# Kernel tuning notes

Measured on AMD Instinct MI355X. Metric: run time of the kernel, lower is better.

## Reference

```python
import jax, jax.numpy as jnp
import numpy as np

I_, J_, D_IN, D_H = 100, 8, 768, 64
N_NODES, N_HE, N_INC, N_CELLS, VOCAB = 160000, 320000, 1600000, 800, 30000
BN_EPS = 1e-5


def setup_inputs() -> dict:
    key = jax.random.key(0)
    ks = jax.random.split(key, 20)
    w = lambda k, s: jax.random.normal(k, s, jnp.float32) * 0.05
    inp = {}
    inp['x'] = jax.random.normal(ks[0], (I_, J_, D_IN), jnp.float32)
    inp['node_tokens'] = jax.random.randint(ks[1], (N_NODES,), 0, VOCAB)
    inp['inc_node'] = jax.random.randint(ks[2], (N_INC,), 0, N_NODES)
    inp['inc_hedge'] = jnp.sort(jax.random.randint(ks[3], (N_INC,), 0, N_HE))
    inp['node2cell'] = jnp.sort(jax.random.randint(ks[4], (N_NODES,), 0, N_CELLS))
    inp['vac_emb'] = w(ks[5], (VOCAB, D_IN))
    inp['fhi_w'] = w(ks[6], (D_IN, D_H)); inp['fhi_b'] = jnp.zeros((D_H,), jnp.float32)
    inp['fin_w'] = w(ks[7], (D_IN, D_H)); inp['fin_b'] = jnp.zeros((D_H,), jnp.float32)
    inp['th1'] = w(ks[8], (D_H, D_H)); inp['b1'] = jnp.zeros((D_H,), jnp.float32)
    inp['th2'] = w(ks[9], (D_H, D_H)); inp['b2'] = jnp.zeros((D_H,), jnp.float32)
    for li, k in zip((1, 2, 3), (ks[10], ks[11], ks[12])):
        inp[f'wc{li}'] = w(k, (D_H, D_H, 3))
        inp[f'bc{li}'] = jnp.zeros((D_H,), jnp.float32)
        inp[f'g{li}'] = jnp.ones((D_H,), jnp.float32)
        inp[f'be{li}'] = jnp.zeros((D_H,), jnp.float32)
        inp[f'm{li}'] = jnp.zeros((D_H,), jnp.float32)
        inp[f'v{li}'] = jnp.ones((D_H,), jnp.float32)
    inp['fct_w'] = w(ks[13], (D_H, D_H)); inp['fct_b'] = jnp.zeros((D_H,), jnp.float32)
    return inp


def _inv_safe(c):
    return jnp.where(c > 0, 1.0 / jnp.maximum(c, 1.0), 0.0)


def _hconv(xf, inc_node, inc_hedge, theta, bias):
    # PyG HypergraphConv (no attention): D^{-1} H W B^{-1} H^T (X Theta) + bias
    xt = xf @ theta                                        # [N, D]
    ones = jnp.ones((inc_node.shape[0],), xt.dtype)
    deg_e = jax.ops.segment_sum(ones, inc_hedge, N_HE)     # B_e
    he = jax.ops.segment_sum(xt[inc_node], inc_hedge, N_HE) * _inv_safe(deg_e)[:, None]
    deg_v = jax.ops.segment_sum(ones, inc_node, N_NODES)   # D_v
    out = jax.ops.segment_sum(he[inc_hedge], inc_node, N_NODES) * _inv_safe(deg_v)[:, None]
    return out + bias


def _conv_bn(h, wc, bc, g, be, m, v):
    # Conv1d(k=3, pad=1) -> ReLU -> BatchNorm1d (inference stats); dropout is eval-mode identity
    h = jax.lax.conv_general_dilated(h, wc, (1,), [(1, 1)],
                                     dimension_numbers=('NCH', 'OIH', 'NCH')) + bc[None, :, None]
    h = jax.nn.relu(h)
    return (h - m[None, :, None]) * (g[None, :, None] / jnp.sqrt(v[None, :, None] + BN_EPS)) + be[None, :, None]


def _forward(x, node_tokens, inc_node, inc_hedge, node2cell, vac_emb, fhi_w, fhi_b,
             fin_w, fin_b, th1, b1, th2, b2, wc1, bc1, g1, be1, m1, v1,
             wc2, bc2, g2, be2, m2, v2, wc3, bc3, g3, be3, m3, v3, fct_w, fct_b):
    # x = fin(x)
    x0 = jnp.einsum('ijd,dh->ijh', x, fin_w) + fin_b       # [100, 8, 64]
    # node_features = fhi(graph_embedding[graph.x])  (gather-dominated)
    nf = vac_emb[node_tokens] @ fhi_w + fhi_b              # [N, 64]
    # two HypergraphConv layers with residuals (eval-mode dropout = identity)
    h1 = jax.nn.relu(_hconv(nf, inc_node, inc_hedge, th1, b1)) + nf
    gx = jax.nn.relu(_hconv(h1, inc_node, inc_hedge, th2, b2)) + nf
    # per-graph mean + max pooling (graph.batch is all-zero per graph => one vector per cell)
    cnt = jax.ops.segment_sum(jnp.ones((N_NODES,), gx.dtype), node2cell, N_CELLS)
    mean_p = jax.ops.segment_sum(gx, node2cell, N_CELLS) * _inv_safe(cnt)[:, None]
    max_p = jax.ops.segment_max(gx, node2cell, N_CELLS)
    max_p = jnp.where(cnt[:, None] > 0, max_p, 0.0)
    cell_emb = 0.5 * (mean_p + max_p)                      # [800, 64]
    x_upd = x0 + 0.3 * cell_emb.reshape(I_, J_, D_H)       # x[i,j] += 0.3*graph_emb
    h = jnp.transpose(x_upd, (0, 2, 1))                    # [100, 64, 8]
    h = _conv_bn(h, wc1, bc1, g1, be1, m1, v1)
    h = _conv_bn(h, wc2, bc2, g2, be2, m2, v2)
    h = _conv_bn(h, wc3, bc3, g3, be3, m3, v3)
    out2 = jnp.mean(h, axis=2) @ fct_w + fct_b             # [100, 64]
    return x_upd, out2


def reference(x, node_tokens, inc_node, inc_hedge, node2cell, vac_emb, fhi_w, fhi_b,
              fin_w, fin_b, th1, b1, th2, b2, wc1, bc1, g1, be1, m1, v1,
              wc2, bc2, g2, be2, m2, v2, wc3, bc3, g3, be3, m3, v3, fct_w, fct_b):
    return _forward(x, node_tokens, inc_node, inc_hedge, node2cell, vac_emb, fhi_w, fhi_b,
                    fin_w, fin_b, th1, b1, th2, b2, wc1, bc1, g1, be1, m1, v1,
                    wc2, bc2, g2, be2, m2, v2, wc3, bc3, g3, be3, m3, v3, fct_w, fct_b)
```

## Files before the change

kernel.cpp:

```cpp
#include <hip/hip_runtime.h>
#include <hip/hip_bf16.h>
#include <cstdint>
#include <cstddef>

#define I_      100
#define J_      8
#define D_IN    768
#define D_H     64
#define N_NODES 160000
#define N_HE    320000
#define N_INC   1600000
#define N_CELLS 800
#define VOCAB   30000

#define NRANGE   256
#define NPR      625
#define SLAB     8192
#define NCHUNK   1000
#define EPB      (N_INC / NCHUNK)

typedef unsigned short u16;
using short8 = __attribute__((ext_vector_type(8))) short;
using f32x4  = __attribute__((ext_vector_type(4))) float;

__device__ __forceinline__ float bf2f(u16 u) {
    union { uint32_t i; float f; } x; x.i = ((uint32_t)u) << 16; return x.f;
}
__device__ __forceinline__ u16 f2bf(float f) {
    union { float f; uint32_t i; } x; x.f = f;
    uint32_t b = x.i;
    b += 0x7FFFu + ((b >> 16) & 1u);
    return (u16)(b >> 16);
}
__device__ __forceinline__ float lo_bf(uint32_t u) {
    union { uint32_t i; float f; } x; x.i = u << 16; return x.f;
}
__device__ __forceinline__ float hi_bf(uint32_t u) {
    union { uint32_t i; float f; } x; x.i = u & 0xFFFF0000u; return x.f;
}
__device__ __forceinline__ uint32_t pack_bf2(float a, float b) {
    return (uint32_t)f2bf(a) | ((uint32_t)f2bf(b) << 16);
}

#define G_OFF_HE   (N_INC / 256)
#define G_OFF_CELL (N_NODES / 256)
#define G_CONV_BIG ((D_IN * 64) / 256)
#define G_CONV_SM  ((64 * 64) / 256)
#define G_KA       NCHUNK
#define G_KB1      256
#define G_KC       NCHUNK
#define G_KD       256
#define G_PGEMM    ((VOCAB + 63) / 64)
#define G_XT       (N_NODES / 64)
#define G_X0       ((I_ * J_ + 63) / 64)
#define G_HEDGE    (N_HE / 32)
#define G_NODE     (N_NODES / 32)

__device__ __forceinline__ void dev_offsets(int bid, const int* __restrict__ sorted,
                                            int n, int nbins, int* __restrict__ off) {
    int i = bid * 256 + threadIdx.x;
    if (i >= n) return;
    int cur = sorted[i];
    int prev = (i == 0) ? -1 : sorted[i - 1];
    for (int b = prev + 1; b <= cur; ++b) off[b] = i;
    if (i == n - 1) {
        for (int b = cur + 1; b <= nbins; ++b) off[b] = n;
    }
}

__device__ __forceinline__ void dev_convT(int bid, const float* __restrict__ B,
                                          u16* __restrict__ Bt, int K) {
    int g = bid * 256 + threadIdx.x;
    if (g >= K * 64) return;
    int k = g >> 6, n = g & 63;
    Bt[(size_t)n * K + k] = f2bf(B[g]);
}

__device__ __forceinline__ void dev_ka(int bid, const int* __restrict__ inc_node,
                                       int* __restrict__ counts, int* __restrict__ lds) {
    int tid = threadIdx.x;
    lds[tid] = 0;
    __syncthreads();
    int s = bid * EPB, e = s + EPB;
    for (int i = s + tid; i < e; i += 256)
        atomicAdd(&lds[(unsigned)inc_node[i] / NPR], 1);
    __syncthreads();
    counts[bid * NRANGE + tid] = lds[tid];
}

__device__ __forceinline__ void dev_kb1(int r, const int* __restrict__ counts,
                                        int* __restrict__ chunk_off,
                                        int* __restrict__ range_total,
                                        int* __restrict__ lds) {
    int tid = threadIdx.x;
    int c0 = tid * 4;
    int v0 = (c0     < NCHUNK) ? counts[(c0    ) * NRANGE + r] : 0;
    int v1 = (c0 + 1 < NCHUNK) ? counts[(c0 + 1) * NRANGE + r] : 0;
    int v2 = (c0 + 2 < NCHUNK) ? counts[(c0 + 2) * NRANGE + r] : 0;
    int v3 = (c0 + 3 < NCHUNK) ? counts[(c0 + 3) * NRANGE + r] : 0;
    int s = v0 + v1 + v2 + v3;
    lds[tid] = s;
    __syncthreads();
    #pragma unroll
    for (int d = 1; d < 256; d <<= 1) {
        int t = (tid >= d) ? lds[tid - d] : 0;
        __syncthreads();
        lds[tid] += t;
        __syncthreads();
    }
    int run = lds[tid] - s;
    if (c0     < NCHUNK) { chunk_off[(c0    ) * NRANGE + r] = run; run += v0; }
    if (c0 + 1 < NCHUNK) { chunk_off[(c0 + 1) * NRANGE + r] = run; run += v1; }
    if (c0 + 2 < NCHUNK) { chunk_off[(c0 + 2) * NRANGE + r] = run; run += v2; }
    if (c0 + 3 < NCHUNK) { chunk_off[(c0 + 3) * NRANGE + r] = run; run += v3; }
    if (tid == 255) range_total[r] = lds[255];
}

__device__ __forceinline__ void dev_kc(int bid, const int* __restrict__ inc_node,
                                       const int* __restrict__ inc_hedge,
                                       const int* __restrict__ chunk_off,
                                       int2* __restrict__ bucket, int* __restrict__ lds) {
    int tid = threadIdx.x;
    int* co  = lds;
    int* cur = lds + 256;
    co[tid]  = tid * SLAB + chunk_off[bid * NRANGE + tid];
    cur[tid] = 0;
    __syncthreads();
    int s = bid * EPB, e = s + EPB;
    for (int i = s + tid; i < e; i += 256) {
        int v = inc_node[i];
        int h = inc_hedge[i];
        int rg = (unsigned)v / NPR;
        int rank = atomicAdd(&cur[rg], 1);
        bucket[co[rg] + rank] = make_int2(v, h);
    }
}

__device__ __forceinline__ void dev_kd(int r, const int2* __restrict__ bucket,
                                       const int* __restrict__ range_total,
                                       int* __restrict__ node_off, int* __restrict__ node_deg,
                                       int* __restrict__ csr, int* __restrict__ lds) {
    int tid = threadIdx.x;
    int* hist = lds;
    int* tsum = lds + 768;
    int* cur  = lds + 1024;
    for (int i = tid; i < 768; i += 256) { hist[i] = 0; cur[i] = 0; }
    __syncthreads();
    int lo = r * NPR;
    int pb = r * SLAB;
    int pe = pb + range_total[r];
    for (int i = pb + tid; i < pe; i += 256)
        atomicAdd(&hist[bucket[i].x - lo], 1);
    __syncthreads();
    int b3 = tid * 3;
    int a0 = hist[b3], a1 = hist[b3 + 1], a2 = hist[b3 + 2];
    int s = a0 + a1 + a2;
    tsum[tid] = s;
    __syncthreads();
    #pragma unroll
    for (int d = 1; d < 256; d <<= 1) {
        int t = (tid >= d) ? tsum[tid - d] : 0;
        __syncthreads();
        tsum[tid] += t;
        __syncthreads();
    }
    int excl = tsum[tid] - s;
    hist[b3]     = excl;
    hist[b3 + 1] = excl + a0;
    hist[b3 + 2] = excl + a0 + a1;
    __syncthreads();
    for (int v = tid; v < NPR; v += 256) {
        int h0 = hist[v];
        node_off[lo + v] = pb + h0;
        node_deg[lo + v] = hist[v + 1] - h0;
    }
    for (int i = pb + tid; i < pe; i += 256) {
        int2 p = bucket[i];
        int l = p.x - lo;
        int k = atomicAdd(&cur[l], 1);
        csr[pb + hist[l] + k] = p.y;
    }
}

template <int BF16_OUT, int GATHER, int KK>
__device__ __forceinline__ void dev_gemm_direct(int wid, const float* __restrict__ A,
                                                const int* __restrict__ tok,
                                                const u16* __restrict__ Bt,
                                                const float* __restrict__ bias,
                                                void* __restrict__ C, int M) {
    int lane = threadIdx.x & 63;
    int m16 = lane & 15, q = lane >> 4;
    int base = wid << 4;
    if (base >= M) return;
    int row = base + m16;
    const float* arow = GATHER ? (A + ((size_t)tok[row] << 6))
                               : (A + (size_t)row * KK);

    f32x4 acc0 = {0.f, 0.f, 0.f, 0.f};
    f32x4 acc1 = {0.f, 0.f, 0.f, 0.f};
    f32x4 acc2 = {0.f, 0.f, 0.f, 0.f};
    f32x4 acc3 = {0.f, 0.f, 0.f, 0.f};

    #pragma unroll 2
    for (int kt = 0; kt < KK; kt += 32) {
        const float* ap = arow + kt + q * 8;
        float4 av0 = *reinterpret_cast<const float4*>(ap);
        float4 av1 = *reinterpret_cast<const float4*>(ap + 4);
        short8 a;
        a[0] = (short)f2bf(av0.x); a[1] = (short)f2bf(av0.y);
        a[2] = (short)f2bf(av0.z); a[3] = (short)f2bf(av0.w);
        a[4] = (short)f2bf(av1.x); a[5] = (short)f2bf(av1.y);
        a[6] = (short)f2bf(av1.z); a[7] = (short)f2bf(av1.w);
        const u16* bp = Bt + (size_t)m16 * KK + kt + q * 8;
        short8 b0 = *reinterpret_cast<const short8*>(bp);
        short8 b1 = *reinterpret_cast<const short8*>(bp + (size_t)16 * KK);
        short8 b2 = *reinterpret_cast<const short8*>(bp + (size_t)32 * KK);
        short8 b3 = *reinterpret_cast<const short8*>(bp + (size_t)48 * KK);
        acc0 = __builtin_amdgcn_mfma_f32_16x16x32_bf16(a, b0, acc0, 0, 0, 0);
        acc1 = __builtin_amdgcn_mfma_f32_16x16x32_bf16(a, b1, acc1, 0, 0, 0);
        acc2 = __builtin_amdgcn_mfma_f32_16x16x32_bf16(a, b2, acc2, 0, 0, 0);
        acc3 = __builtin_amdgcn_mfma_f32_16x16x32_bf16(a, b3, acc3, 0, 0, 0);
    }

    f32x4 accs[4] = {acc0, acc1, acc2, acc3};
    #pragma unroll
    for (int r = 0; r < 4; ++r) {
        int gr = base + q * 4 + r;
        #pragma unroll
        for (int j = 0; j < 4; ++j) {
            int col = j * 16 + m16;
            float v = accs[j][r];
            if (!BF16_OUT) v += bias[col];
            if (BF16_OUT)
                ((u16*)C)[(size_t)gr * 64 + col] = f2bf(v);
            else
                ((float*)C)[(size_t)gr * 64 + col] = v;
        }
    }
}

__device__ __forceinline__ void dev_hedge_sum(int bid, const int* __restrict__ inc_node,
                                              const int* __restrict__ he_off,
                                              const u16* __restrict__ xt,
                                              u16* __restrict__ he) {
    int w = (bid * 256 + (int)threadIdx.x) >> 6;
    int lane = threadIdx.x & 63;
    int sub = lane >> 3;
    int c8 = (lane & 7) << 3;
    int hedge = w * 8 + sub;
    if (hedge >= N_HE) return;
    int s = he_off[hedge], e = he_off[hedge + 1];

    float a0 = 0.f, a1 = 0.f, a2 = 0.f, a3 = 0.f;
    float a4 = 0.f, a5 = 0.f, a6 = 0.f, a7 = 0.f;
    float b0 = 0.f, b1 = 0.f, b2 = 0.f, b3 = 0.f;
    float b4 = 0.f, b5 = 0.f, b6 = 0.f, b7 = 0.f;

    int j = s;
    if ((e - s) & 1) {
        uint4 d = *reinterpret_cast<const uint4*>(xt + (((size_t)inc_node[j]) << 6) + c8);
        a0 += lo_bf(d.x); a1 += hi_bf(d.x);
        a2 += lo_bf(d.y); a3 += hi_bf(d.y);
        a4 += lo_bf(d.z); a5 += hi_bf(d.z);
        a6 += lo_bf(d.w); a7 += hi_bf(d.w);
        ++j;
    }
    int i0 = 0, i1 = 0;
    if (j < e) { i0 = inc_node[j]; i1 = inc_node[j + 1]; }
    for (; j < e; j += 2) {
        int c0 = i0, c1 = i1;
        if (j + 2 < e) { i0 = inc_node[j + 2]; i1 = inc_node[j + 3]; }
        uint4 d0 = *reinterpret_cast<const uint4*>(xt + (((size_t)c0) << 6) + c8);
        uint4 d1 = *reinterpret_cast<const uint4*>(xt + (((size_t)c1) << 6) + c8);
        a0 += lo_bf(d0.x); a1 += hi_bf(d0.x);
        a2 += lo_bf(d0.y); a3 += hi_bf(d0.y);
        a4 += lo_bf(d0.z); a5 += hi_bf(d0.z);
        a6 += lo_bf(d0.w); a7 += hi_bf(d0.w);
        b0 += lo_bf(d1.x); b1 += hi_bf(d1.x);
        b2 += lo_bf(d1.y); b3 += hi_bf(d1.y);
        b4 += lo_bf(d1.z); b5 += hi_bf(d1.z);
        b6 += lo_bf(d1.w); b7 += hi_bf(d1.w);
    }
    a0 += b0; a1 += b1; a2 += b2; a3 += b3;
    a4 += b4; a5 += b5; a6 += b6; a7 += b7;

    float inv = (e > s) ? 1.f / (float)(e - s) : 0.f;
    uint4 o;
    o.x = pack_bf2(a0 * inv, a1 * inv);
    o.y = pack_bf2(a2 * inv, a3 * inv);
    o.z = pack_bf2(a4 * inv, a5 * inv);
    o.w = pack_bf2(a6 * inv, a7 * inv);
    *reinterpret_cast<uint4*>(he + (((size_t)hedge) << 6) + c8) = o;
}

__device__ __forceinline__ void dev_node_sum(int bid, const int* __restrict__ csr,
                                             const int* __restrict__ node_off,
                                             const int* __restrict__ node_deg,
                                             const u16* __restrict__ he,
                                             const float* __restrict__ bias,
                                             const float* __restrict__ P,
                                             const int* __restrict__ tok,
                                             float* __restrict__ out) {
    int w = (bid * 256 + (int)threadIdx.x) >> 6;
    int lane = threadIdx.x & 63;
    int sub = lane >> 3;
    int c8 = (lane & 7) << 3;
    int node = w * 8 + sub;
    if (node >= N_NODES) return;
    int s = node_off[node];
    int e = s + node_deg[node];

    float a0 = 0.f, a1 = 0.f, a2 = 0.f, a3 = 0.f;
    float a4 = 0.f, a5 = 0.f, a6 = 0.f, a7 = 0.f;
    float b0 = 0.f, b1 = 0.f, b2 = 0.f, b3 = 0.f;
    float b4 = 0.f, b5 = 0.f, b6 = 0.f, b7 = 0.f;

    int j = s;
    if ((e - s) & 1) {
        uint4 d = *reinterpret_cast<const uint4*>(he + (((size_t)csr[j]) << 6) + c8);
        a0 += lo_bf(d.x); a1 += hi_bf(d.x);
        a2 += lo_bf(d.y); a3 += hi_bf(d.y);
        a4 += lo_bf(d.z); a5 += hi_bf(d.z);
        a6 += lo_bf(d.w); a7 += hi_bf(d.w);
        ++j;
    }
    int i0 = 0, i1 = 0;
    if (j < e) { i0 = csr[j]; i1 = csr[j + 1]; }
    for (; j < e; j += 2) {
        int c0 = i0, c1 = i1;
        if (j + 2 < e) { i0 = csr[j + 2]; i1 = csr[j + 3]; }
        uint4 d0 = *reinterpret_cast<const uint4*>(he + (((size_t)c0) << 6) + c8);
        uint4 d1 = *reinterpret_cast<const uint4*>(he + (((size_t)c1) << 6) + c8);
        a0 += lo_bf(d0.x); a1 += hi_bf(d0.x);
        a2 += lo_bf(d0.y); a3 += hi_bf(d0.y);
        a4 += lo_bf(d0.z); a5 += hi_bf(d0.z);
        a6 += lo_bf(d0.w); a7 += hi_bf(d0.w);
        b0 += lo_bf(d1.x); b1 += hi_bf(d1.x);
        b2 += lo_bf(d1.y); b3 += hi_bf(d1.y);
        b4 += lo_bf(d1.z); b5 += hi_bf(d1.z);
        b6 += lo_bf(d1.w); b7 += hi_bf(d1.w);
    }
    a0 += b0; a1 += b1; a2 += b2; a3 += b3;
    a4 += b4; a5 += b5; a6 += b6; a7 += b7;

    float inv = (e > s) ? 1.f / (float)(e - s) : 0.f;
    const float* nfp = P + (((size_t)tok[node]) << 6) + c8;
    float4 nv0 = *reinterpret_cast<const float4*>(nfp);
    float4 nv1 = *reinterpret_cast<const float4*>(nfp + 4);
    float4 o0, o1;
    o0.x = fmaxf(fmaf(a0, inv, bias[c8 + 0]), 0.f) + nv0.x;
    o0.y = fmaxf(fmaf(a1, inv, bias[c8 + 1]), 0.f) + nv0.y;
    o0.z = fmaxf(fmaf(a2, inv, bias[c8 + 2]), 0.f) + nv0.z;
    o0.w = fmaxf(fmaf(a3, inv, bias[c8 + 3]), 0.f) + nv0.w;
    o1.x = fmaxf(fmaf(a4, inv, bias[c8 + 4]), 0.f) + nv1.x;
    o1.y = fmaxf(fmaf(a5, inv, bias[c8 + 5]), 0.f) + nv1.y;
    o1.z = fmaxf(fmaf(a6, inv, bias[c8 + 6]), 0.f) + nv1.z;
    o1.w = fmaxf(fmaf(a7, inv, bias[c8 + 7]), 0.f) + nv1.w;
    float* op = out + (((size_t)node) << 6) + c8;
    *reinterpret_cast<float4*>(op) = o0;
    *reinterpret_cast<float4*>(op + 4) = o1;
}

__global__ __launch_bounds__(256) void k_p0(const float* __restrict__ fhi_w,
                                            const float* __restrict__ fin_w,
                                            const float* __restrict__ th1,
                                            const float* __restrict__ th2,
                                            u16* __restrict__ Bt_fhi, u16* __restrict__ Bt_fin,
                                            u16* __restrict__ Bt_th1, u16* __restrict__ Bt_th2,
                                            const int* __restrict__ inc_node,
                                            int* __restrict__ counts) {
    __shared__ int lds[256];
    int bid = blockIdx.x;
    if (bid < G_KA) { dev_ka(bid, inc_node, counts, lds); return; }
    bid -= G_KA;
    if (bid < G_CONV_BIG) { dev_convT(bid, fhi_w, Bt_fhi, D_IN); return; }
    bid -= G_CONV_BIG;
    if (bid < G_CONV_BIG) { dev_convT(bid, fin_w, Bt_fin, D_IN); return; }
    bid -= G_CONV_BIG;
    if (bid < G_CONV_SM) { dev_convT(bid, th1, Bt_th1, 64); return; }
    bid -= G_CONV_SM;
    dev_convT(bid, th2, Bt_th2, 64);
}

__global__ __launch_bounds__(256) void k_p1(const float* __restrict__ vac_emb,
                                            const u16* __restrict__ Bt_fhi,
                                            const float* __restrict__ fhi_b, float* __restrict__ P,
                                            const int* __restrict__ counts,
                                            int* __restrict__ chunk_off, int* __restrict__ range_total,
                                            const int* __restrict__ inc_hedge,
                                            const int* __restrict__ node2cell,
                                            int* __restrict__ he_off, int* __restrict__ cell_off) {
    __shared__ int lds[256];
    int bid = blockIdx.x;
    if (bid < G_KB1) { dev_kb1(bid, counts, chunk_off, range_total, lds); return; }
    bid -= G_KB1;
    if (bid < G_PGEMM) {
        int wid = bid * 4 + ((int)threadIdx.x >> 6);
        dev_gemm_direct<0, 0, D_IN>(wid, vac_emb, nullptr, Bt_fhi, fhi_b, P, VOCAB);
        return;
    }
    bid -= G_PGEMM;
    if (bid < G_OFF_HE) { dev_offsets(bid, inc_hedge, N_INC, N_HE, he_off); return; }
    bid -= G_OFF_HE;
    dev_offsets(bid, node2cell, N_NODES, N_CELLS, cell_off);
}

__global__ __launch_bounds__(256) void k_p2(const float* __restrict__ P,
                                            const int* __restrict__ tok,
                                            const u16* __restrict__ Bt_th1, u16* __restrict__ xt,
                                            const float* __restrict__ x, const u16* __restrict__ Bt_fin,
                                            const float* __restrict__ fin_b, float* __restrict__ x0,
                                            const int* __restrict__ inc_node,
                                            const int* __restrict__ inc_hedge,
                                            const int* __restrict__ chunk_off,
                                            int2* __restrict__ bucket) {
    __shared__ int lds[512];
    int bid = blockIdx.x;
    if (bid < G_KC) { dev_kc(bid, inc_node, inc_hedge, chunk_off, bucket, lds); return; }
    bid -= G_KC;
    if (bid < G_XT) {
        int wid = bid * 4 + ((int)threadIdx.x >> 6);
        dev_gemm_direct<1, 1, 64>(wid, P, tok, Bt_th1, nullptr, xt, N_NODES);
        return;
    }
    bid -= G_XT;
    {
        int wid = bid * 4 + ((int)threadIdx.x >> 6);
        dev_gemm_direct<0, 0, D_IN>(wid, x, nullptr, Bt_fin, fin_b, x0, I_ * J_);
    }
}

__global__ __launch_bounds__(256) void k_p3(const int* __restrict__ inc_node,
                                            const int* __restrict__ he_off,
                                            const u16* __restrict__ xt, u16* __restrict__ he,
                                            const int2* __restrict__ bucket,
                                            const int* __restrict__ range_total,
                                            int* __restrict__ node_off, int* __restrict__ node_deg,
                                            int* __restrict__ csr) {
    __shared__ int lds[1792];
    int bid = blockIdx.x;
    if (bid < G_KD) { dev_kd(bid, bucket, range_total, node_off, node_deg, csr, lds); return; }
    bid -= G_KD;
    dev_hedge_sum(bid, inc_node, he_off, xt, he);
}

__global__ __launch_bounds__(256) void k_xt2(const float* __restrict__ A,
                                             const u16* __restrict__ Bt,
                                             u16* __restrict__ xt) {
    int wid = blockIdx.x * 4 + ((int)threadIdx.x >> 6);
    dev_gemm_direct<1, 0, 64>(wid, A, nullptr, Bt, nullptr, xt, N_NODES);
}

__global__ __launch_bounds__(256) void k_hedge_sum(const int* __restrict__ inc_node,
                                                   const int* __restrict__ he_off,
                                                   const u16* __restrict__ xt,
                                                   u16* __restrict__ he) {
    dev_hedge_sum(blockIdx.x, inc_node, he_off, xt, he);
}

__global__ __launch_bounds__(256) void k_node_sum(const int* __restrict__ csr,
                                                  const int* __restrict__ node_off,
                                                  const int* __restrict__ node_deg,
                                                  const u16* __restrict__ he,
                                                  const float* __restrict__ bias,
                                                  const float* __restrict__ P,
                                                  const int* __restrict__ tok,
                                                  float* __restrict__ out) {
    dev_node_sum(blockIdx.x, csr, node_off, node_deg, he, bias, P, tok, out);
}

__global__ __launch_bounds__(256) void k_pool(const float* __restrict__ gx,
                                              const int* __restrict__ cell_off,
                                              const float* __restrict__ x0,
                                              float* __restrict__ out1) {
    __shared__ float ssum[4][64];
    __shared__ float smax[4][64];
    int c = blockIdx.x;
    int lane = threadIdx.x & 63;
    int w = threadIdx.x >> 6;
    int s = cell_off[c], e = cell_off[c + 1];
    float sum = 0.f, mx = -INFINITY;
    for (int n = s + w; n < e; n += 4) {
        float v = gx[((size_t)n << 6) + lane];
        sum += v;
        mx = fmaxf(mx, v);
    }
    ssum[w][lane] = sum;
    smax[w][lane] = mx;
    __syncthreads();
    if (w == 0) {
        sum = ssum[0][lane] + ssum[1][lane] + ssum[2][lane] + ssum[3][lane];
        mx = fmaxf(fmaxf(smax[0][lane], smax[1][lane]), fmaxf(smax[2][lane], smax[3][lane]));
        int cnt = e - s;
        float mean = (cnt > 0) ? sum / (float)cnt : 0.f;
        float mp = (cnt > 0) ? mx : 0.f;
        float ce = 0.5f * (mean + mp);
        out1[((size_t)c << 6) + lane] = x0[((size_t)c << 6) + lane] + 0.3f * ce;
    }
}

__global__ __launch_bounds__(256) void k_tcn(
    const float* __restrict__ xu,
    const float* __restrict__ wc1, const float* __restrict__ bc1, const float* __restrict__ g1,
    const float* __restrict__ be1, const float* __restrict__ m1, const float* __restrict__ v1,
    const float* __restrict__ wc2, const float* __restrict__ bc2, const float* __restrict__ g2,
    const float* __restrict__ be2, const float* __restrict__ m2, const float* __restrict__ v2,
    const float* __restrict__ wc3, const float* __restrict__ bc3, const float* __restrict__ g3,
    const float* __restrict__ be3, const float* __restrict__ m3, const float* __restrict__ v3,
    const float* __restrict__ fct_w, const float* __restrict__ fct_b,
    float* __restrict__ out2) {
    __shared__ float w_lds[64 * 64 * 3];
    __shared__ float hA[64][10];
    __shared__ float hB[64][10];
    __shared__ float mo[64];

    int n = blockIdx.x, tid = threadIdx.x;

    if (tid < 64) {
        hA[tid][0] = 0.f; hA[tid][9] = 0.f;
        hB[tid][0] = 0.f; hB[tid][9] = 0.f;
    }
    #pragma unroll
    for (int l = tid; l < 512; l += 256) {
        int t = l >> 6, i = l & 63;
        hA[i][t + 1] = xu[(size_t)n * 512 + l];
    }

    const float* wcs[3] = {wc1, wc2, wc3};
    const float* bcs[3] = {bc1, bc2, bc3};
    const float* gs[3]  = {g1, g2, g3};
    const float* bes[3] = {be1, be2, be3};
    const float* ms[3]  = {m1, m2, m3};
    const float* vs[3]  = {v1, v2, v3};

    float (*hin)[10] = hA;
    float (*hout)[10] = hB;

    #pragma unroll
    for (int li = 0; li < 3; ++li) {
        for (int l = tid; l < 64 * 64 * 3; l += 256) w_lds[l] = wcs[li][l];
        __syncthreads();
        #pragma unroll
        for (int rep = 0; rep < 2; ++rep) {
            int idx = tid + rep * 256;
            int o = idx >> 3, t = idx & 7;
            float acc = bcs[li][o];
            #pragma unroll 8
            for (int i = 0; i < 64; ++i) {
                const float* wr = &w_lds[o * 192 + i * 3];
                acc = fmaf(hin[i][t + 0], wr[0], acc);
                acc = fmaf(hin[i][t + 1], wr[1], acc);
                acc = fmaf(hin[i][t + 2], wr[2], acc);
            }
            acc = fmaxf(acc, 0.f);
            float sc = gs[li][o] * rsqrtf(vs[li][o] + 1e-5f);
            acc = (acc - ms[li][o]) * sc + bes[li][o];
            hout[o][t + 1] = acc;
        }
        __syncthreads();
        float (*tmp)[10] = hin; hin = hout; hout = tmp;
    }

    if (tid < 64) {
        float s = 0.f;
        #pragma unroll
        for (int t = 0; t < 8; ++t) s += hin[tid][t + 1];
        mo[tid] = s * 0.125f;
    }
    __syncthreads();
    if (tid < 64) {
        float acc = fct_b[tid];
        #pragma unroll 8
        for (int o = 0; o < 64; ++o) acc = fmaf(mo[o], fct_w[o * 64 + tid], acc);
        out2[(size_t)n * 64 + tid] = acc;
    }
}

extern "C" void kernel_launch(void* const* d_in, const int* in_sizes, int n_in,
                              void* d_out, int out_size, void* d_ws, size_t ws_size,
                              hipStream_t stream) {
    (void)in_sizes; (void)n_in; (void)out_size; (void)ws_size;

    const float* x          = (const float*)d_in[0];
    const int*   node_tok   = (const int*)d_in[1];
    const int*   inc_node   = (const int*)d_in[2];
    const int*   inc_hedge  = (const int*)d_in[3];
    const int*   node2cell  = (const int*)d_in[4];
    const float* vac_emb    = (const float*)d_in[5];
    const float* fhi_w      = (const float*)d_in[6];
    const float* fhi_b      = (const float*)d_in[7];
    const float* fin_w      = (const float*)d_in[8];
    const float* fin_b      = (const float*)d_in[9];
    const float* th1        = (const float*)d_in[10];
    const float* b1         = (const float*)d_in[11];
    const float* th2        = (const float*)d_in[12];
    const float* b2         = (const float*)d_in[13];
    const float* fct_w      = (const float*)d_in[32];
    const float* fct_b      = (const float*)d_in[33];

    char* ws = (char*)d_ws;
    size_t off = 0;
    float* P        = (float*)(ws + off); off += (size_t)VOCAB * 64 * 4;
    float* hbuf     = (float*)(ws + off); off += (size_t)N_NODES * 64 * 4;
    u16*   xt       = (u16*)(ws + off);   off += (size_t)N_NODES * 64 * 2;
    u16*   he       = (u16*)(ws + off);   off += (size_t)N_HE * 64 * 2;
    int2*  bucket   = (int2*)(ws + off);  off += (size_t)NRANGE * SLAB * 8;
    int*   csr      = (int*)(ws + off);   off += (size_t)NRANGE * SLAB * 4;
    float* x0       = (float*)(ws + off); off += (size_t)N_CELLS * 64 * 4;
    u16*   Bt_fhi   = (u16*)(ws + off);   off += (size_t)64 * D_IN * 2;
    u16*   Bt_fin   = (u16*)(ws + off);   off += (size_t)64 * D_IN * 2;
    u16*   Bt_th1   = (u16*)(ws + off);   off += (size_t)64 * 64 * 2;
    u16*   Bt_th2   = (u16*)(ws + off);   off += (size_t)64 * 64 * 2;
    int*   he_off   = (int*)(ws + off);   off += ((size_t)(N_HE + 1) * 4 + 255) / 256 * 256;
    int*   node_off = (int*)(ws + off);   off += (size_t)N_NODES * 4;
    int*   node_deg = (int*)(ws + off);   off += (size_t)N_NODES * 4;
    int*   cell_off = (int*)(ws + off);   off += ((size_t)(N_CELLS + 1) * 4 + 255) / 256 * 256;

    int*  counts      = (int*)hbuf;
    int*  chunk_off   = counts + NCHUNK * NRANGE;
    int*  range_total = chunk_off + NCHUNK * NRANGE;

    float* out1 = (float*)d_out;
    float* out2 = out1 + (size_t)I_ * J_ * D_H;

    k_p0<<<G_KA + 2 * G_CONV_BIG + 2 * G_CONV_SM, 256, 0, stream>>>(
        fhi_w, fin_w, th1, th2, Bt_fhi, Bt_fin, Bt_th1, Bt_th2,
        inc_node, counts);

    k_p1<<<G_KB1 + G_PGEMM + G_OFF_HE + G_OFF_CELL, 256, 0, stream>>>(
        vac_emb, Bt_fhi, fhi_b, P, counts, chunk_off, range_total,
        inc_hedge, node2cell, he_off, cell_off);

    k_p2<<<G_KC + G_XT + G_X0, 256, 0, stream>>>(
        P, node_tok, Bt_th1, xt, x, Bt_fin, fin_b, x0,
        inc_node, inc_hedge, chunk_off, bucket);

    k_p3<<<G_KD + G_HEDGE, 256, 0, stream>>>(inc_node, he_off, xt, he,
                                             bucket, range_total, node_off, node_deg, csr);

    k_node_sum<<<G_NODE, 256, 0, stream>>>(csr, node_off, node_deg, he, b1, P, node_tok, hbuf);

    k_xt2<<<G_XT, 256, 0, stream>>>(hbuf, Bt_th2, xt);

    k_hedge_sum<<<G_HEDGE, 256, 0, stream>>>(inc_node, he_off, xt, he);

    k_node_sum<<<G_NODE, 256, 0, stream>>>(csr, node_off, node_deg, he, b2, P, node_tok, hbuf);

    k_pool<<<N_CELLS, 256, 0, stream>>>(hbuf, cell_off, x0, out1);

    k_tcn<<<I_, 256, 0, stream>>>(out1,
        (const float*)d_in[14], (const float*)d_in[15], (const float*)d_in[16],
        (const float*)d_in[17], (const float*)d_in[18], (const float*)d_in[19],
        (const float*)d_in[20], (const float*)d_in[21], (const float*)d_in[22],
        (const float*)d_in[23], (const float*)d_in[24], (const float*)d_in[25],
        (const float*)d_in[26], (const float*)d_in[27], (const float*)d_in[28],
        (const float*)d_in[29], (const float*)d_in[30], (const float*)d_in[31],
        fct_w, fct_b, out2);
}
```

Before: 502.8 us.

## Fuse first node aggregation with theta2 GEMM and fold pooling into TCN kernel

The first node-sum now packs its 32 rows per block into LDS as bf16 and runs the 64x64 theta2 projection with MFMA in the same kernel, writing xt directly. This skips the fp32 hbuf round trip and the separate GEMM launch. Cell pooling (mean+max) also moves into the TCN kernel, which removes the k_pool launch. The catch is that the pooling loop now runs serially per wave over about 200 nodes per cell with only 100 blocks, so that phase has much less parallelism than the 800-block pool kernel it replaces.

```diff
diff --git a/kernel.cpp b/kernel.cpp
--- a/kernel.cpp
+++ b/kernel.cpp
@@ -55,6 +55,7 @@
 #define G_X0       ((I_ * J_ + 63) / 64)
 #define G_HEDGE    (N_HE / 32)
 #define G_NODE     (N_NODES / 32)
+#define G_NXT      (N_NODES / 32)
 
 __device__ __forceinline__ void dev_offsets(int bid, const int* __restrict__ sorted,
                                             int n, int nbins, int* __restrict__ off) {
@@ -293,20 +294,14 @@
     *reinterpret_cast<uint4*>(he + (((size_t)hedge) << 6) + c8) = o;
 }
 
-__device__ __forceinline__ void dev_node_sum(int bid, const int* __restrict__ csr,
-                                             const int* __restrict__ node_off,
-                                             const int* __restrict__ node_deg,
-                                             const u16* __restrict__ he,
-                                             const float* __restrict__ bias,
-                                             const float* __restrict__ P,
-                                             const int* __restrict__ tok,
-                                             float* __restrict__ out) {
-    int w = (bid * 256 + (int)threadIdx.x) >> 6;
-    int lane = threadIdx.x & 63;
-    int sub = lane >> 3;
-    int c8 = (lane & 7) << 3;
-    int node = w * 8 + sub;
-    if (node >= N_NODES) return;
+__device__ __forceinline__ void dev_node_core(int node, const int* __restrict__ csr,
+                                              const int* __restrict__ node_off,
+                                              const int* __restrict__ node_deg,
+                                              const u16* __restrict__ he,
+                                              const float* __restrict__ bias,
+                                              const float* __restrict__ P,
+                                              const int* __restrict__ tok,
+                                              int c8, float* __restrict__ o) {
     int s = node_off[node];
     int e = s + node_deg[node];
 
@@ -347,16 +342,97 @@
     const float* nfp = P + (((size_t)tok[node]) << 6) + c8;
     float4 nv0 = *reinterpret_cast<const float4*>(nfp);
     float4 nv1 = *reinterpret_cast<const float4*>(nfp + 4);
-    float4 o0, o1;
-    o0.x = fmaxf(fmaf(a0, inv, bias[c8 + 0]), 0.f) + nv0.x;
-    o0.y = fmaxf(fmaf(a1, inv, bias[c8 + 1]), 0.f) + nv0.y;
-    o0.z = fmaxf(fmaf(a2, inv, bias[c8 + 2]), 0.f) + nv0.z;
-    o0.w = fmaxf(fmaf(a3, inv, bias[c8 + 3]), 0.f) + nv0.w;
-    o1.x = fmaxf(fmaf(a4, inv, bias[c8 + 4]), 0.f) + nv1.x;
-    o1.y = fmaxf(fmaf(a5, inv, bias[c8 + 5]), 0.f) + nv1.y;
-    o1.z = fmaxf(fmaf(a6, inv, bias[c8 + 6]), 0.f) + nv1.z;
-    o1.w = fmaxf(fmaf(a7, inv, bias[c8 + 7]), 0.f) + nv1.w;
+    o[0] = fmaxf(fmaf(a0, inv, bias[c8 + 0]), 0.f) + nv0.x;
+    o[1] = fmaxf(fmaf(a1, inv, bias[c8 + 1]), 0.f) + nv0.y;
+    o[2] = fmaxf(fmaf(a2, inv, bias[c8 + 2]), 0.f) + nv0.z;
+    o[3] = fmaxf(fmaf(a3, inv, bias[c8 + 3]), 0.f) + nv0.w;
+    o[4] = fmaxf(fmaf(a4, inv, bias[c8 + 4]), 0.f) + nv1.x;
+    o[5] = fmaxf(fmaf(a5, inv, bias[c8 + 5]), 0.f) + nv1.y;
+    o[6] = fmaxf(fmaf(a6, inv, bias[c8 + 6]), 0.f) + nv1.z;
+    o[7] = fmaxf(fmaf(a7, inv, bias[c8 + 7]), 0.f) + nv1.w;
+}
+
+__global__ __launch_bounds__(256) void k_node_xt(const int* __restrict__ csr,
+                                                 const int* __restrict__ node_off,
+                                                 const int* __restrict__ node_deg,
+                                                 const u16* __restrict__ he,
+                                                 const float* __restrict__ bias,
+                                                 const float* __restrict__ P,
+                                                 const int* __restrict__ tok,
+                                                 const u16* __restrict__ Bt,
+                                                 u16* __restrict__ xt) {
+    __shared__ u16 h1s[32][72];
+    int tid = threadIdx.x;
+    int w = tid >> 6;
+    int lane = tid & 63;
+    int sub = lane >> 3;
+    int c8 = (lane & 7) << 3;
+    int rowib = w * 8 + sub;
+    int node = blockIdx.x * 32 + rowib;
+
+    float o[8];
+    dev_node_core(node, csr, node_off, node_deg, he, bias, P, tok, c8, o);
+
+    uint4 pk;
+    pk.x = pack_bf2(o[0], o[1]);
+    pk.y = pack_bf2(o[2], o[3]);
+    pk.z = pack_bf2(o[4], o[5]);
+    pk.w = pack_bf2(o[6], o[7]);
+    *reinterpret_cast<uint4*>(&h1s[rowib][c8]) = pk;
+    __syncthreads();
+
+    if (w < 2) {
+        int m16 = lane & 15, q = lane >> 4;
+        int base = w * 16;
+        f32x4 acc0 = {0.f, 0.f, 0.f, 0.f};
+        f32x4 acc1 = {0.f, 0.f, 0.f, 0.f};
+        f32x4 acc2 = {0.f, 0.f, 0.f, 0.f};
+        f32x4 acc3 = {0.f, 0.f, 0.f, 0.f};
+        #pragma unroll
+        for (int kt = 0; kt < 64; kt += 32) {
+            short8 a = *reinterpret_cast<const short8*>(&h1s[base + m16][kt + q * 8]);
+            const u16* bp = Bt + (size_t)m16 * 64 + kt + q * 8;
+            short8 b0 = *reinterpret_cast<const short8*>(bp);
+            short8 b1 = *reinterpret_cast<const short8*>(bp + (size_t)16 * 64);
+            short8 b2 = *reinterpret_cast<const short8*>(bp + (size_t)32 * 64);
+            short8 b3 = *reinterpret_cast<const short8*>(bp + (size_t)48 * 64);
+            acc0 = __builtin_amdgcn_mfma_f32_16x16x32_bf16(a, b0, acc0, 0, 0, 0);
+            acc1 = __builtin_amdgcn_mfma_f32_16x16x32_bf16(a, b1, acc1, 0, 0, 0);
+            acc2 = __builtin_amdgcn_mfma_f32_16x16x32_bf16(a, b2, acc2, 0, 0, 0);
+            acc3 = __builtin_amdgcn_mfma_f32_16x16x32_bf16(a, b3, acc3, 0, 0, 0);
+        }
+        f32x4 accs[4] = {acc0, acc1, acc2, acc3};
+        #pragma unroll
+        for (int r = 0; r < 4; ++r) {
+            int gr = blockIdx.x * 32 + base + q * 4 + r;
+            #pragma unroll
+            for (int jj = 0; jj < 4; ++jj) {
+                int col = jj * 16 + m16;
+                xt[(size_t)gr * 64 + col] = f2bf(accs[jj][r]);
+            }
+        }
+    }
+}
+
+__global__ __launch_bounds__(256) void k_node_sum(const int* __restrict__ csr,
+                                                  const int* __restrict__ node_off,
+                                                  const int* __restrict__ node_deg,
+                                                  const u16* __restrict__ he,
+                                                  const float* __restrict__ bias,
+                                                  const float* __restrict__ P,
+                                                  const int* __restrict__ tok,
+                                                  float* __restrict__ out) {
+    int w = (blockIdx.x * 256 + (int)threadIdx.x) >> 6;
+    int lane = threadIdx.x & 63;
+    int sub = lane >> 3;
+    int c8 = (lane & 7) << 3;
+    int node = w * 8 + sub;
+    if (node >= N_NODES) return;
+    float o[8];
+    dev_node_core(node, csr, node_off, node_deg, he, bias, P, tok, c8, o);
     float* op = out + (((size_t)node) << 6) + c8;
+    float4 o0 = make_float4(o[0], o[1], o[2], o[3]);
+    float4 o1 = make_float4(o[4], o[5], o[6], o[7]);
     *reinterpret_cast<float4*>(op) = o0;
     *reinterpret_cast<float4*>(op + 4) = o1;
 }
@@ -444,13 +520,6 @@
     dev_hedge_sum(bid, inc_node, he_off, xt, he);
 }
 
-__global__ __launch_bounds__(256) void k_xt2(const float* __restrict__ A,
-                                             const u16* __restrict__ Bt,
-                                             u16* __restrict__ xt) {
-    int wid = blockIdx.x * 4 + ((int)threadIdx.x >> 6);
-    dev_gemm_direct<1, 0, 64>(wid, A, nullptr, Bt, nullptr, xt, N_NODES);
-}
-
 __global__ __launch_bounds__(256) void k_hedge_sum(const int* __restrict__ inc_node,
                                                    const int* __restrict__ he_off,
                                                    const u16* __restrict__ xt,
@@ -458,49 +527,9 @@
     dev_hedge_sum(blockIdx.x, inc_node, he_off, xt, he);
 }
 
-__global__ __launch_bounds__(256) void k_node_sum(const int* __restrict__ csr,
-                                                  const int* __restrict__ node_off,
-                                                  const int* __restrict__ node_deg,
-                                                  const u16* __restrict__ he,
-                                                  const float* __restrict__ bias,
-                                                  const float* __restrict__ P,
-                                                  const int* __restrict__ tok,
-                                                  float* __restrict__ out) {
-    dev_node_sum(blockIdx.x, csr, node_off, node_deg, he, bias, P, tok, out);
-}
-
-__global__ __launch_bounds__(256) void k_pool(const float* __restrict__ gx,
-                                              const int* __restrict__ cell_off,
-                                              const float* __restrict__ x0,
-                                              float* __restrict__ out1) {
-    __shared__ float ssum[4][64];
-    __shared__ float smax[4][64];
-    int c = blockIdx.x;
-    int lane = threadIdx.x & 63;
-    int w = threadIdx.x >> 6;
-    int s = cell_off[c], e = cell_off[c + 1];
-    float sum = 0.f, mx = -INFINITY;
-    for (int n = s + w; n < e; n += 4) {
-        float v = gx[((size_t)n << 6) + lane];
-        sum += v;
-        mx = fmaxf(mx, v);
-    }
-    ssum[w][lane] = sum;
-    smax[w][lane] = mx;
-    __syncthreads();
-    if (w == 0) {
-        sum = ssum[0][lane] + ssum[1][lane] + ssum[2][lane] + ssum[3][lane];
-        mx = fmaxf(fmaxf(smax[0][lane], smax[1][lane]), fmaxf(smax[2][lane], smax[3][lane]));
-        int cnt = e - s;
-        float mean = (cnt > 0) ? sum / (float)cnt : 0.f;
-        float mp = (cnt > 0) ? mx : 0.f;
-        float ce = 0.5f * (mean + mp);
-        out1[((size_t)c << 6) + lane] = x0[((size_t)c << 6) + lane] + 0.3f * ce;
-    }
-}
-
 __global__ __launch_bounds__(256) void k_tcn(
-    const float* __restrict__ xu,
+    const float* __restrict__ gx, const int* __restrict__ cell_off,
+    const float* __restrict__ x0, float* __restrict__ out1,
     const float* __restrict__ wc1, const float* __restrict__ bc1, const float* __restrict__ g1,
     const float* __restrict__ be1, const float* __restrict__ m1, const float* __restrict__ v1,
     const float* __restrict__ wc2, const float* __restrict__ bc2, const float* __restrict__ g2,
@@ -515,15 +544,32 @@
     __shared__ float mo[64];
 
     int n = blockIdx.x, tid = threadIdx.x;
+    int lane = tid & 63;
+    int w = tid >> 6;
 
     if (tid < 64) {
         hA[tid][0] = 0.f; hA[tid][9] = 0.f;
         hB[tid][0] = 0.f; hB[tid][9] = 0.f;
     }
+
     #pragma unroll
-    for (int l = tid; l < 512; l += 256) {
-        int t = l >> 6, i = l & 63;
-        hA[i][t + 1] = xu[(size_t)n * 512 + l];
+    for (int tt = 0; tt < 2; ++tt) {
+        int t = w * 2 + tt;
+        int c = n * 8 + t;
+        int s = cell_off[c], e = cell_off[c + 1];
+        float sum = 0.f, mx = -INFINITY;
+        for (int nd = s; nd < e; ++nd) {
+            float v = gx[(((size_t)nd) << 6) + lane];
+            sum += v;
+            mx = fmaxf(mx, v);
+        }
+        int cnt = e - s;
+        float mean = (cnt > 0) ? sum / (float)cnt : 0.f;
+        float mp = (cnt > 0) ? mx : 0.f;
+        float ce = 0.5f * (mean + mp);
+        float xv = x0[(((size_t)c) << 6) + lane] + 0.3f * ce;
+        out1[(((size_t)c) << 6) + lane] = xv;
+        hA[lane][t + 1] = xv;
     }
 
     const float* wcs[3] = {wc1, wc2, wc3};
@@ -638,17 +684,14 @@
     k_p3<<<G_KD + G_HEDGE, 256, 0, stream>>>(inc_node, he_off, xt, he,
                                              bucket, range_total, node_off, node_deg, csr);
 
-    k_node_sum<<<G_NODE, 256, 0, stream>>>(csr, node_off, node_deg, he, b1, P, node_tok, hbuf);
-
-    k_xt2<<<G_XT, 256, 0, stream>>>(hbuf, Bt_th2, xt);
+    k_node_xt<<<G_NXT, 256, 0, stream>>>(csr, node_off, node_deg, he, b1, P, node_tok,
+                                         Bt_th2, xt);
 
     k_hedge_sum<<<G_HEDGE, 256, 0, stream>>>(inc_node, he_off, xt, he);
 
     k_node_sum<<<G_NODE, 256, 0, stream>>>(csr, node_off, node_deg, he, b2, P, node_tok, hbuf);
 
-    k_pool<<<N_CELLS, 256, 0, stream>>>(hbuf, cell_off, x0, out1);
-
-    k_tcn<<<I_, 256, 0, stream>>>(out1,
+    k_tcn<<<I_, 256, 0, stream>>>(hbuf, cell_off, x0, out1,
         (const float*)d_in[14], (const float*)d_in[15], (const float*)d_in[16],
         (const float*)d_in[17], (const float*)d_in[18], (const float*)d_in[19],
         (const float*)d_in[20], (const float*)d_in[21], (const float*)d_in[22],
```

Result: slower. 578.3 us (+15.0%).
